# Kernel optimization log

Measured on AMD Instinct MI355X. Metric: run time of the kernel, lower is better.

The kernel has to match this reference:

```python
import jax, jax.numpy as jnp
import numpy as np

B, S, D, H = 1, 4096, 1024, 16
HD = D // H  # head_dim = 64


def setup_inputs() -> dict:
    key = jax.random.key(0)
    k1, k2, k3 = jax.random.split(key, 3)
    scale = 0.02
    return {
        "x": jax.random.normal(k1, (B, S, D), dtype=jnp.float32),
        "w_qkv": jax.random.normal(k2, (D, 3 * D), dtype=jnp.float32) * scale,
        "b_qkv": jnp.zeros((3 * D,), dtype=jnp.float32),
        "w_proj": jax.random.normal(k3, (D, D), dtype=jnp.float32) * scale,
        "b_proj": jnp.zeros((D,), dtype=jnp.float32),
    }


def reference(x, w_qkv, b_qkv, w_proj, b_proj):
    b, s, d = x.shape
    qkv = x @ w_qkv + b_qkv                      # [b, s, 3d]
    q, k, v = jnp.split(qkv, 3, axis=-1)
    # [b, h, s, hd]
    q = q.reshape(b, s, H, HD).transpose(0, 2, 1, 3)
    k = k.reshape(b, s, H, HD).transpose(0, 2, 1, 3)
    v = v.reshape(b, s, H, HD).transpose(0, 2, 1, 3)
    score = jnp.einsum("bhqd,bhkd->bhqk", q, k) / jnp.sqrt(jnp.float32(HD))
    causal = jnp.tril(jnp.ones((s, s), dtype=bool))
    score = jnp.where(causal, score, -jnp.inf)
    attn = jax.nn.softmax(score, axis=-1)        # dropout omitted (eval mode, p effectively 0)
    out = jnp.einsum("bhqk,bhkd->bhqd", attn, v)  # [b, h, s, hd]
    out = out.transpose(0, 2, 1, 3).reshape(b, s, d)
    return out @ w_proj + b_proj
```

## Files before the change

kernel.cpp:

```cpp
#include <hip/hip_runtime.h>
#include <hip/hip_bf16.h>
#include <math.h>

typedef __bf16 bf16;
typedef __bf16 bf16x8 __attribute__((ext_vector_type(8)));
typedef __bf16 bf16x4 __attribute__((ext_vector_type(4)));
typedef float f32x4 __attribute__((ext_vector_type(4)));

#define S_ 4096
#define D_ 1024
#define H_ 16
#define HD_ 64
#define N3_ 3072
#define NSPLIT 4

typedef const __attribute__((address_space(1))) void* gas1_t;
typedef __attribute__((address_space(3))) void* las3_t;
static __device__ __forceinline__ void g2l16(const void* g, void* l) {
  __builtin_amdgcn_global_load_lds((gas1_t)g, (las3_t)l, 16, 0, 0);
}

__global__ __launch_bounds__(256) void prep_kernel(const float* __restrict__ x,
                                                   bf16* __restrict__ xb,
                                                   const float* __restrict__ w_qkv,
                                                   bf16* __restrict__ wqkvT,
                                                   const float* __restrict__ w_proj,
                                                   bf16* __restrict__ wprojT) {
  __shared__ float t[32][33];
  const int b = blockIdx.x;
  if (b < 4096) {
    int i = (b * 256 + threadIdx.x) * 4;
    float4 v = *(const float4*)(x + i);
    bf16x4 o;
    o.x = (bf16)v.x; o.y = (bf16)v.y; o.z = (bf16)v.z; o.w = (bf16)v.w;
    *(bf16x4*)(xb + i) = o;
    return;
  }
  const float* in; bf16* outp; int ldin, bx, by;
  if (b < 7168) { int b2 = b - 4096; in = w_qkv;  outp = wqkvT;  ldin = N3_; bx = (b2 % 96) * 32; by = (b2 / 96) * 32; }
  else          { int b3 = b - 7168; in = w_proj; outp = wprojT; ldin = D_;  bx = (b3 % 32) * 32; by = (b3 / 32) * 32; }
  const int tx = threadIdx.x & 31, ty = threadIdx.x >> 5;
#pragma unroll
  for (int i = 0; i < 4; ++i)
    t[ty + i * 8][tx] = in[(size_t)(by + ty + i * 8) * ldin + bx + tx];
  __syncthreads();
#pragma unroll
  for (int i = 0; i < 4; ++i)
    outp[(size_t)(bx + ty + i * 8) * D_ + by + tx] = (bf16)t[tx][ty + i * 8];
}

template <int BN>
__global__ __launch_bounds__(256) void gemm_bt(const bf16* __restrict__ A,
                                               const bf16* __restrict__ Bt,
                                               const float* __restrict__ bias,
                                               bf16* __restrict__ outb,
                                               float* __restrict__ outf,
                                               bf16* __restrict__ vTout,
                                               int M, int N, int K,
                                               int qlim, float qscale) {
  constexpr int NT = BN / 32;
  __shared__ bf16 sA[128 * 32];
  __shared__ bf16 sB[BN * 32];
  const int tid = threadIdx.x;
  const int wave = tid >> 6, lane = tid & 63;
  const int col = lane & 15, quad = lane >> 4;
  const int wm = (wave & 1) * 64, wn = (wave >> 1) * (BN / 2);
  const long bm = (long)blockIdx.x * 128, bn = (long)blockIdx.y * BN;
  const int srow = tid >> 2;
  const int soff = (tid & 3) * 8;

  f32x4 acc[4][NT] = {};

  for (int kb = 0; kb < K; kb += 32) {
    __syncthreads();
    g2l16(A + (bm + srow) * (long)K + kb + soff,      &sA[tid * 8]);
    g2l16(A + (bm + 64 + srow) * (long)K + kb + soff, &sA[2048 + tid * 8]);
#pragma unroll
    for (int i = 0; i < BN / 64; ++i)
      g2l16(Bt + (bn + i * 64 + srow) * (long)K + kb + soff, &sB[i * 2048 + tid * 8]);
    __syncthreads();

    bf16x8 af[4], bfr[NT];
#pragma unroll
    for (int t = 0; t < 4; ++t)
      af[t] = *(const bf16x8*)(&sA[(wm + t * 16 + col) * 32 + quad * 8]);
#pragma unroll
    for (int t = 0; t < NT; ++t)
      bfr[t] = *(const bf16x8*)(&sB[(wn + t * 16 + col) * 32 + quad * 8]);
#pragma unroll
    for (int mt = 0; mt < 4; ++mt)
#pragma unroll
      for (int nt = 0; nt < NT; ++nt)
        acc[mt][nt] = __builtin_amdgcn_mfma_f32_16x16x32_bf16(af[mt], bfr[nt], acc[mt][nt], 0, 0, 0);
  }

#pragma unroll
  for (int mt = 0; mt < 4; ++mt) {
#pragma unroll
    for (int nt = 0; nt < NT; ++nt) {
      long gn = bn + wn + nt * 16 + col;
      float bv = bias ? bias[gn] : 0.f;
      if (vTout && gn >= 2 * D_) {
        bf16x4 vv;
        long gm0 = bm + wm + mt * 16 + quad * 4;
#pragma unroll
        for (int i = 0; i < 4; ++i) vv[i] = (bf16)(acc[mt][nt][i] + bv);
        *(bf16x4*)(&vTout[(gn - 2 * D_) * (long)S_ + gm0]) = vv;
      } else {
        float sc = (gn < qlim) ? qscale : 1.0f;
#pragma unroll
        for (int i = 0; i < 4; ++i) {
          long gm = bm + wm + mt * 16 + quad * 4 + i;
          float v = (acc[mt][nt][i] + bv) * sc;
          if (outf) outf[gm * N + gn] = v;
          else      outb[gm * N + gn] = (bf16)v;
        }
      }
    }
  }
}

__device__ __forceinline__ int swz_g(int row) {
  return (row & 3) | ((((row >> 2) ^ (row >> 3)) & 1) << 2);
}

__global__ __launch_bounds__(256) void attn_kernel(const bf16* __restrict__ qkv,
                                                   const bf16* __restrict__ vT,
                                                   bf16* __restrict__ Opart,
                                                   float* __restrict__ lws) {
  __shared__ bf16 sK[2][64 * 64];
  __shared__ bf16 sV[2][64 * 64];
  const int hh = blockIdx.x;
  const int qb = (int)(gridDim.y - 1 - blockIdx.y);
  const int sp = blockIdx.z;
  const int tid = threadIdx.x;
  const int wave = tid >> 6, lane = tid & 63;
  const int col = lane & 15, quad = lane >> 4;
  const int qbase = qb * 128 + wave * 32;

  const bf16* qp0 = qkv + (size_t)(qbase + col) * N3_ + hh * HD_;
  bf16x8 aq[2][2];
  aq[0][0] = *(const bf16x8*)(qp0 + quad * 8);
  aq[0][1] = *(const bf16x8*)(qp0 + 32 + quad * 8);
  aq[1][0] = *(const bf16x8*)(qp0 + 16 * N3_ + quad * 8);
  aq[1][1] = *(const bf16x8*)(qp0 + 16 * N3_ + 32 + quad * 8);

  bf16x8 ones;
#pragma unroll
  for (int j = 0; j < 8; ++j) ones[j] = (bf16)1.0f;

  f32x4 acc[2][4] = {};
  f32x4 acc_l[2] = {};

  const bf16* kgbase = qkv + D_ + hh * HD_;
  const bf16* vgbase = vT + (size_t)hh * HD_ * S_;
  const int krow = (col >> 2) * 8 + (col & 3);
  const int niter = 2 * (qb + 1);
  const int base = niter >> 2, rem = niter & 3;
  const int it0 = sp * base + (sp < rem ? sp : rem);
  const int len = base + (sp < rem ? 1 : 0);
  const int it1 = it0 + len;

  const int srow = tid >> 2;
  const int sc0 = (tid & 3) * 2;
  const int gs = swz_g(srow);
  const int soff0 = srow * 64 + ((sc0 ^ gs) * 8);
  const int soff1 = srow * 64 + (((sc0 + 1) ^ gs) * 8);

  if (len > 0) {
    {
      const bf16* kg = kgbase + (size_t)(it0 * 64 + srow) * N3_ + sc0 * 8;
      const bf16* vg = vgbase + (size_t)srow * S_ + it0 * 64 + sc0 * 8;
      *(int4*)(&sK[0][soff0]) = *(const int4*)kg;
      *(int4*)(&sK[0][soff1]) = *(const int4*)(kg + 8);
      *(int4*)(&sV[0][soff0]) = *(const int4*)vg;
      *(int4*)(&sV[0][soff1]) = *(const int4*)(vg + 8);
    }
    __syncthreads();

    for (int j = it0; j < it1; ++j) {
      const int kb = j * 64;
      const int cur = (j - it0) & 1;
      const bool more = (j + 1 < it1);
      int4 pk0, pk1, pv0, pv1;
      if (more) {
        const bf16* kg = kgbase + (size_t)(kb + 64 + srow) * N3_ + sc0 * 8;
        const bf16* vg = vgbase + (size_t)srow * S_ + kb + 64 + sc0 * 8;
        pk0 = *(const int4*)kg; pk1 = *(const int4*)(kg + 8);
        pv0 = *(const int4*)vg; pv1 = *(const int4*)(vg + 8);
      }

      if (kb < qbase + 32) {
        const bool act0 = kb < qbase + 16;
        const bf16* kc = &sK[cur][0];
        const bf16* vc = &sV[cur][0];

        f32x4 st[2][4];
#pragma unroll
        for (int t = 0; t < 4; ++t) {
          int row = (t >> 1) * 32 + (t & 1) * 4 + krow;
          int pc = quad ^ swz_g(row);
          bf16x8 bk0 = *(const bf16x8*)(kc + row * 64 + pc * 8);
          bf16x8 bk1 = *(const bf16x8*)(kc + row * 64 + (pc ^ 4) * 8);
          if (act0) {
            f32x4 z = {};
            z = __builtin_amdgcn_mfma_f32_16x16x32_bf16(bk0, aq[0][0], z, 0, 0, 0);
            st[0][t] = __builtin_amdgcn_mfma_f32_16x16x32_bf16(bk1, aq[0][1], z, 0, 0, 0);
          }
          f32x4 z = {};
          z = __builtin_amdgcn_mfma_f32_16x16x32_bf16(bk0, aq[1][0], z, 0, 0, 0);
          st[1][t] = __builtin_amdgcn_mfma_f32_16x16x32_bf16(bk1, aq[1][1], z, 0, 0, 0);
        }

        bf16x8 pfrag[2][2];
#pragma unroll
        for (int s2 = 0; s2 < 2; ++s2) {
          if (s2 == 0 && !act0) continue;
          const int rowbase = qbase + 16 * s2;
          float p[4][4];
          if (kb + 63 <= rowbase) {
#pragma unroll
            for (int t = 0; t < 4; ++t)
#pragma unroll
              for (int r = 0; r < 4; ++r)
                p[t][r] = __builtin_amdgcn_exp2f(st[s2][t][r]);
          } else {
#pragma unroll
            for (int t = 0; t < 4; ++t)
#pragma unroll
              for (int r = 0; r < 4; ++r) {
                int key = kb + (t >> 1) * 32 + quad * 8 + (t & 1) * 4 + r;
                p[t][r] = (key > rowbase + col)
                              ? 0.f
                              : __builtin_amdgcn_exp2f(st[s2][t][r]);
              }
          }
#pragma unroll
          for (int c = 0; c < 2; ++c)
#pragma unroll
            for (int j2 = 0; j2 < 4; ++j2) {
              pfrag[s2][c][j2]     = (bf16)p[2 * c][j2];
              pfrag[s2][c][j2 + 4] = (bf16)p[2 * c + 1][j2];
            }
        }

#pragma unroll
        for (int c = 0; c < 2; ++c) {
#pragma unroll
          for (int n = 0; n < 4; ++n) {
            int row = n * 16 + col;
            int pc = (4 * c + quad) ^ swz_g(row);
            bf16x8 bv = *(const bf16x8*)(vc + row * 64 + pc * 8);
            if (act0)
              acc[0][n] = __builtin_amdgcn_mfma_f32_16x16x32_bf16(pfrag[0][c], bv, acc[0][n], 0, 0, 0);
            acc[1][n] = __builtin_amdgcn_mfma_f32_16x16x32_bf16(pfrag[1][c], bv, acc[1][n], 0, 0, 0);
          }
          if (act0)
            acc_l[0] = __builtin_amdgcn_mfma_f32_16x16x32_bf16(pfrag[0][c], ones, acc_l[0], 0, 0, 0);
          acc_l[1] = __builtin_amdgcn_mfma_f32_16x16x32_bf16(pfrag[1][c], ones, acc_l[1], 0, 0, 0);
        }
      }

      if (more) {
        bf16* kn = &sK[cur ^ 1][0];
        bf16* vn = &sV[cur ^ 1][0];
        *(int4*)(kn + soff0) = pk0;
        *(int4*)(kn + soff1) = pk1;
        *(int4*)(vn + soff0) = pv0;
        *(int4*)(vn + soff1) = pv1;
      }
      __syncthreads();
    }
  }

  bf16* Op = Opart + (size_t)sp * S_ * D_;
#pragma unroll
  for (int s2 = 0; s2 < 2; ++s2) {
    const int rowbase = qbase + 16 * s2;
    if (col == 0) {
#pragma unroll
      for (int r = 0; r < 4; ++r)
        lws[((size_t)sp * H_ + hh) * S_ + rowbase + quad * 4 + r] = acc_l[s2][r];
    }
#pragma unroll
    for (int n = 0; n < 4; ++n)
#pragma unroll
      for (int r = 0; r < 4; ++r)
        Op[(size_t)(rowbase + quad * 4 + r) * D_ + hh * HD_ + n * 16 + col] =
            (bf16)acc[s2][n][r];
  }
}

__global__ __launch_bounds__(256) void attn_combine(const bf16* __restrict__ Opart,
                                                    const float* __restrict__ lws,
                                                    bf16* __restrict__ outb) {
  int e = (blockIdx.x * 256 + threadIdx.x) * 8;
  int s = e >> 10;
  int h = (e & (D_ - 1)) >> 6;
  float l = 0.f;
#pragma unroll
  for (int sp = 0; sp < NSPLIT; ++sp) l += lws[((size_t)sp * H_ + h) * S_ + s];
  float inv = 1.0f / l;
  float o[8] = {};
#pragma unroll
  for (int sp = 0; sp < NSPLIT; ++sp) {
    bf16x8 a = *(const bf16x8*)(Opart + (size_t)sp * S_ * D_ + e);
#pragma unroll
    for (int j = 0; j < 8; ++j) o[j] += (float)a[j];
  }
  bf16x8 r;
#pragma unroll
  for (int j = 0; j < 8; ++j) r[j] = (bf16)(o[j] * inv);
  *(bf16x8*)(outb + e) = r;
}

extern "C" void kernel_launch(void* const* d_in, const int* in_sizes, int n_in,
                              void* d_out, int out_size, void* d_ws, size_t ws_size,
                              hipStream_t stream) {
  const float* x      = (const float*)d_in[0];
  const float* w_qkv  = (const float*)d_in[1];
  const float* b_qkv  = (const float*)d_in[2];
  const float* w_proj = (const float*)d_in[3];
  const float* b_proj = (const float*)d_in[4];
  float* out = (float*)d_out;

  bf16* xb     = (bf16*)d_ws;
  bf16* wqkvT  = xb + (size_t)S_ * D_;
  bf16* wprojT = wqkvT + (size_t)N3_ * D_;
  bf16* qkv    = wprojT + (size_t)D_ * D_;
  bf16* vT     = qkv + (size_t)S_ * N3_;
  bf16* Opart  = vT + (size_t)D_ * S_;
  float* lws   = (float*)(Opart + (size_t)NSPLIT * S_ * D_);
  bf16* attn   = xb;

  const float QSCALE = 0.125f * 1.44269504088896f;

  prep_kernel<<<dim3(8192), 256, 0, stream>>>(x, xb, w_qkv, wqkvT, w_proj, wprojT);
  gemm_bt<128><<<dim3(S_ / 128, N3_ / 128), 256, 0, stream>>>(
      xb, wqkvT, b_qkv, qkv, nullptr, vT, S_, N3_, D_, D_, QSCALE);
  attn_kernel<<<dim3(H_, S_ / 128, NSPLIT), 256, 0, stream>>>(qkv, vT, Opart, lws);
  attn_combine<<<dim3((S_ * D_) / 2048), 256, 0, stream>>>(Opart, lws, attn);
  gemm_bt<64><<<dim3(S_ / 128, D_ / 64), 256, 0, stream>>>(
      attn, wprojT, b_proj, nullptr, out, nullptr, S_, D_, D_, 0, 1.0f);
}
```

Measured before the change: 212.0 us.

## Replace QKV GEMM with 256x256 ping-pong pipelined 8-wave kernel

Adds a dedicated QKV projection GEMM using 256x256 tiles and 512 threads. It uses direct global-to-LDS loads with XOR swizzle, a double-buffered half-tile staging schedule with explicit waitcnt and barriers, and s_setprio around MFMA bursts. The goal is more data reuse per tile and better overlap of loads with MFMA compared with the 128x128 generic gemm_bt. It uses 128KB of LDS, which limits occupancy, and the hand-written vmcnt accounting is fragile.

```diff
diff --git a/kernel.cpp b/kernel.cpp
--- a/kernel.cpp
+++ b/kernel.cpp
@@ -120,6 +120,186 @@
   }
 }
 
+__global__ __launch_bounds__(512, 2) void gemm256_qkv(const bf16* __restrict__ A,
+                                                      const bf16* __restrict__ Bt,
+                                                      const float* __restrict__ bias,
+                                                      bf16* __restrict__ outb,
+                                                      bf16* __restrict__ vTout,
+                                                      float qscale) {
+  __shared__ bf16 smem[65536];
+  const int K = D_;
+  const int NTK = K / 64;
+  const int tid = threadIdx.x;
+  const int lane = tid & 63, wv = tid >> 6;
+  const int col = lane & 15, quad = lane >> 4;
+  const int wr = wv >> 2, wc = wv & 3;
+  const long bm = (long)blockIdx.x * 256, bn = (long)blockIdx.y * 256;
+
+  int srowA[2][2], srowB[2][2];
+  int schA[2][2], schB[2][2];
+#pragma unroll
+  for (int q = 0; q < 2; ++q) {
+    int slot = q * 512 + tid;
+    int rl = slot >> 3, ch = slot & 7;
+#pragma unroll
+    for (int h = 0; h < 2; ++h) {
+      int rowA = (rl & 63) | (h << 6) | ((rl >> 6) << 7);
+      srowA[h][q] = rowA; schA[h][q] = ch ^ (rowA & 7);
+      int rowB = (rl & 31) | (h << 5) | ((rl >> 5) << 6);
+      srowB[h][q] = rowB; schB[h][q] = ch ^ (rowB & 7);
+    }
+  }
+  const int dstoff = tid * 8;
+
+  const int ck[2] = { ((0 * 4 + quad) ^ (col & 7)) * 8, ((1 * 4 + quad) ^ (col & 7)) * 8 };
+
+#define STAGE_A(h, T, buf)                                                        \
+  {                                                                               \
+    const int kbs = (T) * 64;                                                     \
+    bf16* lb = smem + (buf) * 32768 + (h) * 8192;                                 \
+    g2l16(A + (bm + srowA[h][0]) * (long)K + kbs + schA[h][0] * 8, lb + dstoff);  \
+    g2l16(A + (bm + srowA[h][1]) * (long)K + kbs + schA[h][1] * 8, lb + 4096 + dstoff); \
+  }
+#define STAGE_B(h, T, buf)                                                        \
+  {                                                                               \
+    const int kbs = (T) * 64;                                                     \
+    bf16* lb = smem + (buf) * 32768 + 16384 + (h) * 8192;                         \
+    g2l16(Bt + (bn + srowB[h][0]) * (long)K + kbs + schB[h][0] * 8, lb + dstoff); \
+    g2l16(Bt + (bn + srowB[h][1]) * (long)K + kbs + schB[h][1] * 8, lb + 4096 + dstoff); \
+  }
+
+  f32x4 acc[8][4] = {};
+
+  STAGE_A(0, 0, 0);
+  STAGE_A(1, 0, 0);
+  STAGE_B(0, 0, 0);
+  STAGE_A(0, 1, 1);
+  STAGE_B(1, 0, 0);
+
+  for (int G = 0; G < NTK; ++G) {
+    const int cur = G & 1;
+    const bf16* bufc = smem + cur * 32768;
+    const bool last = (G == NTK - 1);
+
+    bf16x8 afr[4][2], bfr[2][2][2];
+
+    if (last) asm volatile("s_waitcnt vmcnt(2)" ::: "memory");
+    else      asm volatile("s_waitcnt vmcnt(4)" ::: "memory");
+    __builtin_amdgcn_s_barrier();
+    __builtin_amdgcn_sched_barrier(0);
+#pragma unroll
+    for (int mt = 0; mt < 4; ++mt) {
+      const bf16* rp = bufc + (wr * 64 + mt * 16 + col) * 64;
+      afr[mt][0] = *(const bf16x8*)(rp + ck[0]);
+      afr[mt][1] = *(const bf16x8*)(rp + ck[1]);
+    }
+#pragma unroll
+    for (int nt = 0; nt < 2; ++nt) {
+      const bf16* rp = bufc + 16384 + (wc * 32 + nt * 16 + col) * 64;
+      bfr[0][nt][0] = *(const bf16x8*)(rp + ck[0]);
+      bfr[0][nt][1] = *(const bf16x8*)(rp + ck[1]);
+    }
+    if (G + 1 < NTK) STAGE_A(1, G + 1, cur ^ 1);
+    asm volatile("s_waitcnt lgkmcnt(0)" ::: "memory");
+    __builtin_amdgcn_sched_barrier(0);
+    __builtin_amdgcn_s_setprio(1);
+#pragma unroll
+    for (int mt = 0; mt < 4; ++mt)
+#pragma unroll
+      for (int nt = 0; nt < 2; ++nt) {
+        acc[mt][nt] = __builtin_amdgcn_mfma_f32_16x16x32_bf16(afr[mt][0], bfr[0][nt][0], acc[mt][nt], 0, 0, 0);
+        acc[mt][nt] = __builtin_amdgcn_mfma_f32_16x16x32_bf16(afr[mt][1], bfr[0][nt][1], acc[mt][nt], 0, 0, 0);
+      }
+    __builtin_amdgcn_s_setprio(0);
+
+    if (last) asm volatile("s_waitcnt vmcnt(0)" ::: "memory");
+    else      asm volatile("s_waitcnt vmcnt(2)" ::: "memory");
+    __builtin_amdgcn_s_barrier();
+    __builtin_amdgcn_sched_barrier(0);
+#pragma unroll
+    for (int nt = 0; nt < 2; ++nt) {
+      const bf16* rp = bufc + 16384 + 8192 + (wc * 32 + nt * 16 + col) * 64;
+      bfr[1][nt][0] = *(const bf16x8*)(rp + ck[0]);
+      bfr[1][nt][1] = *(const bf16x8*)(rp + ck[1]);
+    }
+    if (G + 1 < NTK) STAGE_B(0, G + 1, cur ^ 1);
+    asm volatile("s_waitcnt lgkmcnt(0)" ::: "memory");
+    __builtin_amdgcn_sched_barrier(0);
+    __builtin_amdgcn_s_setprio(1);
+#pragma unroll
+    for (int mt = 0; mt < 4; ++mt)
+#pragma unroll
+      for (int nt = 0; nt < 2; ++nt) {
+        acc[mt][2 + nt] = __builtin_amdgcn_mfma_f32_16x16x32_bf16(afr[mt][0], bfr[1][nt][0], acc[mt][2 + nt], 0, 0, 0);
+        acc[mt][2 + nt] = __builtin_amdgcn_mfma_f32_16x16x32_bf16(afr[mt][1], bfr[1][nt][1], acc[mt][2 + nt], 0, 0, 0);
+      }
+    __builtin_amdgcn_s_setprio(0);
+
+    __builtin_amdgcn_s_barrier();
+    __builtin_amdgcn_sched_barrier(0);
+#pragma unroll
+    for (int mt = 0; mt < 4; ++mt) {
+      const bf16* rp = bufc + 8192 + (wr * 64 + mt * 16 + col) * 64;
+      afr[mt][0] = *(const bf16x8*)(rp + ck[0]);
+      afr[mt][1] = *(const bf16x8*)(rp + ck[1]);
+    }
+    if (G + 2 < NTK) STAGE_A(0, G + 2, cur);
+    asm volatile("s_waitcnt lgkmcnt(0)" ::: "memory");
+    __builtin_amdgcn_sched_barrier(0);
+    __builtin_amdgcn_s_setprio(1);
+#pragma unroll
+    for (int mt = 0; mt < 4; ++mt)
+#pragma unroll
+      for (int nt = 0; nt < 2; ++nt) {
+        acc[4 + mt][2 + nt] = __builtin_amdgcn_mfma_f32_16x16x32_bf16(afr[mt][0], bfr[1][nt][0], acc[4 + mt][2 + nt], 0, 0, 0);
+        acc[4 + mt][2 + nt] = __builtin_amdgcn_mfma_f32_16x16x32_bf16(afr[mt][1], bfr[1][nt][1], acc[4 + mt][2 + nt], 0, 0, 0);
+      }
+    __builtin_amdgcn_s_setprio(0);
+
+    __builtin_amdgcn_s_barrier();
+    __builtin_amdgcn_sched_barrier(0);
+    if (G + 1 < NTK) STAGE_B(1, G + 1, cur ^ 1);
+    __builtin_amdgcn_s_setprio(1);
+#pragma unroll
+    for (int mt = 0; mt < 4; ++mt)
+#pragma unroll
+      for (int nt = 0; nt < 2; ++nt) {
+        acc[4 + mt][nt] = __builtin_amdgcn_mfma_f32_16x16x32_bf16(afr[mt][0], bfr[0][nt][0], acc[4 + mt][nt], 0, 0, 0);
+        acc[4 + mt][nt] = __builtin_amdgcn_mfma_f32_16x16x32_bf16(afr[mt][1], bfr[0][nt][1], acc[4 + mt][nt], 0, 0, 0);
+      }
+    __builtin_amdgcn_s_setprio(0);
+  }
+
+  const bool isV = (blockIdx.y >= 8);
+  const bool isQ = (blockIdx.y < 4);
+#pragma unroll
+  for (int mh = 0; mh < 2; ++mh)
+#pragma unroll
+    for (int mt = 0; mt < 4; ++mt)
+#pragma unroll
+      for (int nh = 0; nh < 2; ++nh)
+#pragma unroll
+        for (int nt = 0; nt < 2; ++nt) {
+          long gn = bn + wc * 64 + nh * 32 + nt * 16 + col;
+          float bv = bias[gn];
+          long gm0 = bm + wr * 128 + mh * 64 + mt * 16 + quad * 4;
+          f32x4 a = acc[mh * 4 + mt][nh * 2 + nt];
+          if (isV) {
+            bf16x4 vv;
+#pragma unroll
+            for (int i = 0; i < 4; ++i) vv[i] = (bf16)(a[i] + bv);
+            *(bf16x4*)(&vTout[(gn - 2 * D_) * (long)S_ + gm0]) = vv;
+          } else {
+            float sc = isQ ? qscale : 1.0f;
+#pragma unroll
+            for (int i = 0; i < 4; ++i)
+              outb[(gm0 + i) * (long)N3_ + gn] = (bf16)((a[i] + bv) * sc);
+          }
+        }
+#undef STAGE_A
+#undef STAGE_B
+}
+
 __device__ __forceinline__ int swz_g(int row) {
   return (row & 3) | ((((row >> 2) ^ (row >> 3)) & 1) << 2);
 }
@@ -336,8 +516,8 @@
   const float QSCALE = 0.125f * 1.44269504088896f;
 
   prep_kernel<<<dim3(8192), 256, 0, stream>>>(x, xb, w_qkv, wqkvT, w_proj, wprojT);
-  gemm_bt<128><<<dim3(S_ / 128, N3_ / 128), 256, 0, stream>>>(
-      xb, wqkvT, b_qkv, qkv, nullptr, vT, S_, N3_, D_, D_, QSCALE);
+  gemm256_qkv<<<dim3(S_ / 256, N3_ / 256), 512, 0, stream>>>(
+      xb, wqkvT, b_qkv, qkv, vT, QSCALE);
   attn_kernel<<<dim3(H_, S_ / 128, NSPLIT), 256, 0, stream>>>(qkv, vT, Opart, lws);
   attn_combine<<<dim3((S_ * D_) / 2048), 256, 0, stream>>>(Opart, lws, attn);
   gemm_bt<64><<<dim3(S_ / 128, D_ / 64), 256, 0, stream>>>(
```

After: 206.6 us. 2.6% less time.
